# Performance work log

Measured on AMD Instinct MI355X. Metric: run time of the kernel, lower is better.

## Reference

```python
import jax, jax.numpy as jnp
import numpy as np

D = 768
H = 8
DH = D // H
SCALE = DH ** -0.5


def layer_norm(x, g, b, eps=1e-5):
    mu = jnp.mean(x, axis=-1, keepdims=True)
    var = jnp.var(x, axis=-1, keepdims=True)
    return (x - mu) * jax.lax.rsqrt(var + eps) * g + b


def setup_inputs() -> dict:
    key = jax.random.key(0)
    ks = jax.random.split(key, 8)
    B, N = 8, 1024
    s = lambda fan_in: 1.0 / np.sqrt(fan_in)
    return {
        "x": jax.random.normal(ks[0], (B, N, D), jnp.float32),
        "w_qkv": jax.random.normal(ks[1], (D, 3 * D), jnp.float32) * s(D),
        "w_o": jax.random.normal(ks[2], (D, D), jnp.float32) * s(D),
        "b_o": jnp.zeros((D,), jnp.float32),
        "w1": jax.random.normal(ks[3], (D, 4 * D), jnp.float32) * s(D),
        "b1": jnp.zeros((4 * D,), jnp.float32),
        "w2": jax.random.normal(ks[4], (4 * D, D), jnp.float32) * s(4 * D),
        "b2": jnp.zeros((D,), jnp.float32),
        "g1": jnp.ones((D,), jnp.float32), "be1": jnp.zeros((D,), jnp.float32),
        "gm": jnp.ones((D,), jnp.float32), "bm": jnp.zeros((D,), jnp.float32),
        "g3": jnp.ones((D,), jnp.float32), "be3": jnp.zeros((D,), jnp.float32),
    }


def reference(x, w_qkv, w_o, b_o, w1, b1, w2, b2, g1, be1, gm, bm, g3, be3):
    B, N, _ = x.shape
    # --- attention branch (pre-norm) ---
    h = layer_norm(x, g1, be1)
    qkv = h @ w_qkv                                   # (B,N,3D)
    qkv = qkv.reshape(B, N, 3, H, DH).transpose(2, 0, 3, 1, 4)  # (3,B,H,N,Dh)
    q, k, v = qkv[0], qkv[1], qkv[2]
    att = jax.nn.softmax(jnp.einsum('bhnd,bhmd->bhnm', q, k) * SCALE, axis=-1)
    o = jnp.einsum('bhnm,bhmd->bhnd', att, v)         # (B,H,N,Dh)
    # faithful to original: reshape WITHOUT transposing heads back
    o = o.reshape(B, N, D)
    o = o @ w_o + b_o
    x = o + x
    # --- MLP branch (has its own pre-norm; GELU after BOTH linears; dropout off) ---
    h = layer_norm(x, gm, bm)
    h = jax.nn.gelu(h @ w1 + b1, approximate=False)
    h = jax.nn.gelu(h @ w2 + b2, approximate=False)
    x = h + x
    return layer_norm(x, g3, be3)
```

## Files before the change

### kernel.cpp

```cpp
#include <hip/hip_runtime.h>
#include <cmath>
#include <cstdint>

typedef __bf16 bf16;
typedef __bf16 bf16x8 __attribute__((ext_vector_type(8)));
typedef __bf16 bf16x4 __attribute__((ext_vector_type(4)));
typedef float  f32x4  __attribute__((ext_vector_type(4)));

#define M_TOK 8192
#define SCALE_ 0.10206207261596575f

__device__ __forceinline__ void gld_lds16(const void* g, void* l) {
  __builtin_amdgcn_global_load_lds(
      (__attribute__((address_space(1))) void*)(uintptr_t)g,
      (__attribute__((address_space(3))) void*)(uintptr_t)l,
      16, 0, 0);
}

__device__ __forceinline__ float gelu_f(float x) {
  float u = x * (0.7978845608f + 0.0356774081f * x * x);
  float t = 1.0f - 2.0f / (__expf(2.0f * u) + 1.0f);
  return 0.5f * x * (1.0f + t);
}

__global__ __launch_bounds__(256) void make_frags_kernel(
    const float* __restrict__ w_qkv, const float* __restrict__ w_o,
    const float* __restrict__ w1, const float* __restrict__ w2,
    bf16* __restrict__ fqkv, bf16* __restrict__ fwo, bf16* __restrict__ fw1,
    bf16* __restrict__ fw2) {
  int chunk = blockIdx.x * 4 + (threadIdx.x >> 6);
  int lane = threadIdx.x & 63;
  const float* src;
  bf16* dst;
  int K, N, base;
  if (chunk < 3456) {
    src = w_qkv; dst = fqkv; K = 768; N = 2304; base = 0;
  } else if (chunk < 4608) {
    src = w_o; dst = fwo; K = 768; N = 768; base = 3456;
  } else if (chunk < 9216) {
    src = w1; dst = fw1; K = 768; N = 3072; base = 4608;
  } else {
    src = w2; dst = fw2; K = 3072; N = 768; base = 9216;
  }
  int lid = chunk - base;
  int kc = K / 32;
  int n16 = lid / kc, c = lid - n16 * kc;
  int lr = lane & 15, qd = lane >> 4;
  int n = n16 * 16 + lr;
  int k0 = c * 32 + qd * 8;
  bf16x8 v;
#pragma unroll
  for (int e = 0; e < 8; e++) v[e] = (bf16)src[(size_t)(k0 + e) * N + n];
  *(bf16x8*)&dst[(size_t)lid * 512 + lane * 8] = v;
}

__global__ __launch_bounds__(256) void ln_kernel(
    const float* __restrict__ x, const float* __restrict__ g,
    const float* __restrict__ b, bf16* __restrict__ ob) {
  int w = threadIdx.x >> 6, lane = threadIdx.x & 63;
  size_t row = (size_t)blockIdx.x * 4 + w;
  const float* xr = x + row * 768;
  float4 v[3];
  float s = 0.f, sq = 0.f;
#pragma unroll
  for (int k = 0; k < 3; k++) {
    v[k] = *(const float4*)(xr + (k * 64 + lane) * 4);
    s += v[k].x + v[k].y + v[k].z + v[k].w;
    sq += v[k].x * v[k].x + v[k].y * v[k].y + v[k].z * v[k].z + v[k].w * v[k].w;
  }
#pragma unroll
  for (int off = 32; off >= 1; off >>= 1) {
    s += __shfl_xor(s, off);
    sq += __shfl_xor(sq, off);
  }
  float mean = s * (1.f / 768.f);
  float rstd = rsqrtf(sq * (1.f / 768.f) - mean * mean + 1e-5f);
#pragma unroll
  for (int k = 0; k < 3; k++) {
    int c = (k * 64 + lane) * 4;
    float4 gg = *(const float4*)(g + c);
    float4 bb = *(const float4*)(b + c);
    bf16x4 pk = {(bf16)((v[k].x - mean) * rstd * gg.x + bb.x),
                 (bf16)((v[k].y - mean) * rstd * gg.y + bb.y),
                 (bf16)((v[k].z - mean) * rstd * gg.z + bb.z),
                 (bf16)((v[k].w - mean) * rstd * gg.w + bb.w)};
    *(bf16x4*)(ob + row * 768 + c) = pk;
  }
}

__global__ __launch_bounds__(256) void ln2_reduce_kernel(
    const bf16* __restrict__ p, const float* __restrict__ bo,
    const float* __restrict__ xres, const float* __restrict__ g,
    const float* __restrict__ b, bf16* __restrict__ x2,
    bf16* __restrict__ h2) {
  int w = threadIdx.x >> 6, lane = threadIdx.x & 63;
  size_t row = (size_t)blockIdx.x * 4 + w;
  const bf16* p0 = p + row * 768;
  const bf16* p1 = p0 + (size_t)M_TOK * 768;
  const float* xr = xres + row * 768;
  float4 v[3];
  float s = 0.f, sq = 0.f;
#pragma unroll
  for (int k = 0; k < 3; k++) {
    int c = (k * 64 + lane) * 4;
    bf16x4 a0 = *(const bf16x4*)(p0 + c);
    bf16x4 a1 = *(const bf16x4*)(p1 + c);
    float4 bb = *(const float4*)(bo + c);
    float4 rr = *(const float4*)(xr + c);
    v[k].x = (float)a0[0] + (float)a1[0] + bb.x + rr.x;
    v[k].y = (float)a0[1] + (float)a1[1] + bb.y + rr.y;
    v[k].z = (float)a0[2] + (float)a1[2] + bb.z + rr.z;
    v[k].w = (float)a0[3] + (float)a1[3] + bb.w + rr.w;
    bf16x4 xo = {(bf16)v[k].x, (bf16)v[k].y, (bf16)v[k].z, (bf16)v[k].w};
    *(bf16x4*)(x2 + row * 768 + c) = xo;
    s += v[k].x + v[k].y + v[k].z + v[k].w;
    sq += v[k].x * v[k].x + v[k].y * v[k].y + v[k].z * v[k].z + v[k].w * v[k].w;
  }
#pragma unroll
  for (int off = 32; off >= 1; off >>= 1) {
    s += __shfl_xor(s, off);
    sq += __shfl_xor(sq, off);
  }
  float mean = s * (1.f / 768.f);
  float rstd = rsqrtf(sq * (1.f / 768.f) - mean * mean + 1e-5f);
#pragma unroll
  for (int k = 0; k < 3; k++) {
    int c = (k * 64 + lane) * 4;
    float4 gg = *(const float4*)(g + c);
    float4 bb = *(const float4*)(b + c);
    bf16x4 pk = {(bf16)((v[k].x - mean) * rstd * gg.x + bb.x),
                 (bf16)((v[k].y - mean) * rstd * gg.y + bb.y),
                 (bf16)((v[k].z - mean) * rstd * gg.z + bb.z),
                 (bf16)((v[k].w - mean) * rstd * gg.w + bb.w)};
    *(bf16x4*)(h2 + row * 768 + c) = pk;
  }
}

__global__ __launch_bounds__(256) void ln3_reduce_kernel(
    const bf16* __restrict__ p, const float* __restrict__ b2,
    const bf16* __restrict__ x2, const float* __restrict__ g,
    const float* __restrict__ b, float* __restrict__ out) {
  int w = threadIdx.x >> 6, lane = threadIdx.x & 63;
  size_t row = (size_t)blockIdx.x * 4 + w;
  const bf16* p0 = p + row * 768;
  const bf16* p1 = p0 + (size_t)M_TOK * 768;
  const bf16* xr = x2 + row * 768;
  float4 v[3];
  float s = 0.f, sq = 0.f;
#pragma unroll
  for (int k = 0; k < 3; k++) {
    int c = (k * 64 + lane) * 4;
    bf16x4 a0 = *(const bf16x4*)(p0 + c);
    bf16x4 a1 = *(const bf16x4*)(p1 + c);
    float4 bb = *(const float4*)(b2 + c);
    bf16x4 rr = *(const bf16x4*)(xr + c);
    v[k].x = gelu_f((float)a0[0] + (float)a1[0] + bb.x) + (float)rr[0];
    v[k].y = gelu_f((float)a0[1] + (float)a1[1] + bb.y) + (float)rr[1];
    v[k].z = gelu_f((float)a0[2] + (float)a1[2] + bb.z) + (float)rr[2];
    v[k].w = gelu_f((float)a0[3] + (float)a1[3] + bb.w) + (float)rr[3];
    s += v[k].x + v[k].y + v[k].z + v[k].w;
    sq += v[k].x * v[k].x + v[k].y * v[k].y + v[k].z * v[k].z + v[k].w * v[k].w;
  }
#pragma unroll
  for (int off = 32; off >= 1; off >>= 1) {
    s += __shfl_xor(s, off);
    sq += __shfl_xor(sq, off);
  }
  float mean = s * (1.f / 768.f);
  float rstd = rsqrtf(sq * (1.f / 768.f) - mean * mean + 1e-5f);
#pragma unroll
  for (int k = 0; k < 3; k++) {
    int c = (k * 64 + lane) * 4;
    float4 gg = *(const float4*)(g + c);
    float4 bb = *(const float4*)(b + c);
    float4 ov = {(v[k].x - mean) * rstd * gg.x + bb.x,
                 (v[k].y - mean) * rstd * gg.y + bb.y,
                 (v[k].z - mean) * rstd * gg.z + bb.z,
                 (v[k].w - mean) * rstd * gg.w + bb.w};
    *(float4*)(out + row * 768 + c) = ov;
  }
}

template <int EPI, int LDA, int KTOT, int KSL, int NN>
__global__ __launch_bounds__(512, 2) void gemm8p_kernel(
    const bf16* __restrict__ A, const bf16* __restrict__ Bf,
    const float* __restrict__ bias, bf16* __restrict__ outb,
    bf16* __restrict__ qo, bf16* __restrict__ ko, bf16* __restrict__ vto) {
  constexpr int KCg = KTOT / 32;
  constexpr int NT = KSL / 64;
  __shared__ __align__(16) bf16 smem[3][24576];
  int tid = threadIdx.x;
  int w = tid >> 6, l = tid & 63;
  int qd = l >> 4, lr = l & 15;
  int bm0 = blockIdx.x * 128, bn0 = blockIdx.y * 256;
  int kbase = blockIdx.z * KSL;
  int wm = (w >> 2) * 64;
  int wnl = (w & 3) * 4;

  int rA = w * 8 + (l >> 3);
  int csA = (l & 7) ^ (l >> 3);
  const bf16* pA =
      A + (size_t)(bm0 + rA) * LDA + kbase + csA * 8;
  const bf16* pB0 =
      Bf + ((size_t)((bn0 >> 4) + (w >> 1)) * KCg + (kbase >> 5) + (w & 1)) *
               512 +
      l * 8;

  auto STG_A = [&](int t, bf16* buf) {
    gld_lds16(pA + t * 64, (char*)buf + w * 1024);
    gld_lds16(pA + t * 64 + (size_t)64 * LDA, (char*)buf + (8 + w) * 1024);
  };
  auto STG_B = [&](int t, bf16* buf, int g) {
    gld_lds16(pB0 + (size_t)g * (4 * KCg * 512) + (size_t)t * 1024,
              (char*)buf + 16384 + (w + 8 * g) * 1024);
  };

  STG_A(0, smem[0]);
  STG_B(0, smem[0], 0); STG_B(0, smem[0], 1);
  STG_B(0, smem[0], 2); STG_B(0, smem[0], 3);
  STG_A(1, smem[1]);
  STG_B(1, smem[1], 0); STG_B(1, smem[1], 1);
  STG_B(1, smem[1], 2); STG_B(1, smem[1], 3);
  asm volatile("s_waitcnt vmcnt(6)" ::: "memory");
  __builtin_amdgcn_sched_barrier(0);
  __builtin_amdgcn_s_barrier();

  f32x4 acc[4][4] = {};

#pragma unroll 1
  for (int kt3 = 0; kt3 < NT; kt3 += 3) {
#pragma unroll
    for (int u = 0; u < 3; ++u) {
      const int kt = kt3 + u;
      const bf16* Ab = smem[u];
      const bf16* Bb = smem[u] + 8192;
      bf16* nbuf = smem[(u + 2) % 3];
      bool st = (kt + 2) < NT;
#pragma unroll
      for (int k2 = 0; k2 < 2; ++k2) {
        bf16x8 af[4], bv[4];
        __builtin_amdgcn_sched_barrier(0);
#pragma unroll
        for (int i = 0; i < 4; ++i)
          af[i] = *(const bf16x8*)(Ab + (wm + i * 16 + lr) * 64 +
                                   (((k2 << 2) | qd) ^ (lr & 7)) * 8);
#pragma unroll
        for (int j = 0; j < 4; ++j)
          bv[j] = *(const bf16x8*)(Bb + (((wnl + j) << 1) | k2) * 512 + l * 8);
        __builtin_amdgcn_sched_barrier(0);
        if (k2 == 0) {
          if (st) { STG_A(kt + 2, nbuf); STG_B(kt + 2, nbuf, 0); }
        } else {
          if (st) {
            STG_B(kt + 2, nbuf, 1);
            STG_B(kt + 2, nbuf, 2);
            STG_B(kt + 2, nbuf, 3);
          }
        }
        __builtin_amdgcn_sched_barrier(0);
        __builtin_amdgcn_s_barrier();
        asm volatile("s_waitcnt lgkmcnt(0)" ::: "memory");
        __builtin_amdgcn_sched_barrier(0);
        __builtin_amdgcn_s_setprio(1);
#pragma unroll
        for (int i = 0; i < 4; ++i)
#pragma unroll
          for (int j = 0; j < 4; ++j)
            acc[i][j] = __builtin_amdgcn_mfma_f32_16x16x32_bf16(
                af[i], bv[j], acc[i][j], 0, 0, 0);
        __builtin_amdgcn_s_setprio(0);
        __builtin_amdgcn_sched_barrier(0);
      }
      if (kt + 1 < NT) {
        if (st) asm volatile("s_waitcnt vmcnt(6)" ::: "memory");
        else    asm volatile("s_waitcnt vmcnt(0)" ::: "memory");
        __builtin_amdgcn_sched_barrier(0);
        __builtin_amdgcn_s_barrier();
      }
    }
  }

  int wn = (w & 3) * 64;
  bf16* outbs = (EPI == 5) ? outb + (size_t)blockIdx.z * M_TOK * NN : outb;

#pragma unroll
  for (int i = 0; i < 4; i++) {
#pragma unroll
    for (int j = 0; j < 4; j++) {
      if (EPI == 4) {
        int colt = bn0 + wn + j * 16;
        int which = colt / 768;
        int rem = colt - which * 768;
        int h = rem / 96;
        int dhb = rem - h * 96;
        int row0 = bm0 + wm + i * 16 + qd * 4;
        int b = row0 >> 10, n0 = row0 & 1023;
        int bh = b * 8 + h;
        if (which == 2) {
          bf16x4 pk = {(bf16)acc[i][j][0], (bf16)acc[i][j][1],
                       (bf16)acc[i][j][2], (bf16)acc[i][j][3]};
          *(bf16x4*)(vto + ((size_t)(bh * 96 + dhb + lr)) * 1024 + n0) = pk;
        } else if (which == 0) {
#pragma unroll
          for (int r = 0; r < 4; r++)
            qo[((size_t)bh * 1024 + n0 + r) * 96 + dhb + lr] =
                (bf16)(acc[i][j][r] * SCALE_);
        } else {
#pragma unroll
          for (int r = 0; r < 4; r++)
            ko[((size_t)bh * 1024 + n0 + r) * 96 + dhb + lr] =
                (bf16)acc[i][j][r];
        }
      } else {
#pragma unroll
        for (int r = 0; r < 4; r++) {
          int row = bm0 + wm + i * 16 + qd * 4 + r;
          int col = bn0 + wn + j * 16 + lr;
          size_t o = (size_t)row * NN + col;
          float v = acc[i][j][r];
          if (EPI == 2) {
            outbs[o] = (bf16)gelu_f(v + bias[col]);
          } else {
            outbs[o] = (bf16)v;
          }
        }
      }
    }
  }
}

__global__ __launch_bounds__(256) void attn_kernel(
    const bf16* __restrict__ qb, const bf16* __restrict__ kb,
    const bf16* __restrict__ vtb, bf16* __restrict__ operm) {
  __shared__ __align__(16) bf16 Ks[2][64 * 104];
  __shared__ __align__(16) bf16 Vs[2][96 * 72];
  __shared__ __align__(16) bf16 Ps[128 * 72];
  int t = threadIdx.x;
  int w = t >> 6, lane = t & 63;
  int qd = lane >> 4, lr = lane & 15;
  int bh = blockIdx.x, nt0 = blockIdx.y * 128;
  int bq = bh >> 3, hh = bh & 7;

  const bf16* kgb = kb + (size_t)bh * 1024 * 96;
  const bf16* vgb = vtb + (size_t)bh * 96 * 1024;

  bf16x8 kreg[3], vreg[3];
#pragma unroll
  for (int it = 0; it < 3; it++) {
    int idx = it * 256 + t;
    kreg[it] = *(const bf16x8*)(kgb + (idx / 12) * 96 + (idx % 12) * 8);
    vreg[it] = *(const bf16x8*)(vgb + (size_t)(idx >> 3) * 1024 + (idx & 7) * 8);
  }

  const bf16* qg = qb + ((size_t)bh * 1024 + nt0 + w * 32) * 96;
  bf16x8 afq[2][3];
#pragma unroll
  for (int i = 0; i < 2; i++)
#pragma unroll
    for (int ks = 0; ks < 3; ks++)
      afq[i][ks] = *(const bf16x8*)(qg + (i * 16 + lr) * 96 + ks * 32 + qd * 8);

  f32x4 oacc[2][6] = {};
  float lst[2][4] = {};

  int cur = 0;
  for (int kt = 0; kt < 16; kt++) {
#pragma unroll
    for (int it = 0; it < 3; it++) {
      int idx = it * 256 + t;
      *(bf16x8*)&Ks[cur][(idx / 12) * 104 + (idx % 12) * 8] = kreg[it];
      *(bf16x8*)&Vs[cur][(idx >> 3) * 72 + (idx & 7) * 8] = vreg[it];
    }
    if (kt < 15) {
      const bf16* kg = kgb + (size_t)(kt + 1) * 64 * 96;
      const bf16* vg = vgb + (kt + 1) * 64;
#pragma unroll
      for (int it = 0; it < 3; it++) {
        int idx = it * 256 + t;
        kreg[it] = *(const bf16x8*)(kg + (idx / 12) * 96 + (idx % 12) * 8);
        vreg[it] =
            *(const bf16x8*)(vg + (size_t)(idx >> 3) * 1024 + (idx & 7) * 8);
      }
    }
    __syncthreads();

    f32x4 sacc[2][4] = {};
#pragma unroll
    for (int ks = 0; ks < 3; ks++) {
      bf16x8 bk[4];
#pragma unroll
      for (int jn = 0; jn < 4; jn++)
        bk[jn] =
            *(const bf16x8*)&Ks[cur][(jn * 16 + lr) * 104 + ks * 32 + qd * 8];
#pragma unroll
      for (int i = 0; i < 2; i++)
#pragma unroll
        for (int jn = 0; jn < 4; jn++)
          sacc[i][jn] = __builtin_amdgcn_mfma_f32_16x16x32_bf16(
              afq[i][ks], bk[jn], sacc[i][jn], 0, 0, 0);
    }

#pragma unroll
    for (int i = 0; i < 2; i++)
#pragma unroll
      for (int jn = 0; jn < 4; jn++)
#pragma unroll
        for (int r = 0; r < 4; r++) {
          float p = __expf(sacc[i][jn][r]);
          lst[i][r] += p;
          Ps[(w * 32 + i * 16 + qd * 4 + r) * 72 + jn * 16 + lr] = (bf16)p;
        }

#pragma unroll
    for (int ks = 0; ks < 2; ks++) {
      bf16x8 ap[2];
#pragma unroll
      for (int i = 0; i < 2; i++)
        ap[i] =
            *(const bf16x8*)&Ps[(w * 32 + i * 16 + lr) * 72 + ks * 32 + qd * 8];
#pragma unroll
      for (int jn = 0; jn < 6; jn++) {
        bf16x8 bv =
            *(const bf16x8*)&Vs[cur][(jn * 16 + lr) * 72 + ks * 32 + qd * 8];
#pragma unroll
        for (int i = 0; i < 2; i++)
          oacc[i][jn] = __builtin_amdgcn_mfma_f32_16x16x32_bf16(
              ap[i], bv, oacc[i][jn], 0, 0, 0);
      }
    }
    cur ^= 1;
  }

#pragma unroll
  for (int i = 0; i < 2; i++)
#pragma unroll
    for (int r = 0; r < 4; r++) {
#pragma unroll
      for (int off = 1; off < 16; off <<= 1)
        lst[i][r] += __shfl_xor(lst[i][r], off);
    }

#pragma unroll
  for (int i = 0; i < 2; i++) {
#pragma unroll
    for (int r = 0; r < 4; r++) {
      float inv = 1.0f / lst[i][r];
      int n = nt0 + w * 32 + i * 16 + qd * 4 + r;
      size_t rowo = (size_t)bq * 1024 + hh * 128 + (n >> 3);
      int colb = 96 * (n & 7);
#pragma unroll
      for (int jn = 0; jn < 6; jn++)
        operm[rowo * 768 + colb + jn * 16 + lr] =
            (bf16)(oacc[i][jn][r] * inv);
    }
  }
}

extern "C" void kernel_launch(void* const* d_in, const int* in_sizes, int n_in,
                              void* d_out, int out_size, void* d_ws,
                              size_t ws_size, hipStream_t stream) {
  const float* x = (const float*)d_in[0];
  const float* w_qkv = (const float*)d_in[1];
  const float* w_o = (const float*)d_in[2];
  const float* b_o = (const float*)d_in[3];
  const float* w1 = (const float*)d_in[4];
  const float* b1 = (const float*)d_in[5];
  const float* w2 = (const float*)d_in[6];
  const float* b2 = (const float*)d_in[7];
  const float* g1 = (const float*)d_in[8];
  const float* be1 = (const float*)d_in[9];
  const float* gm = (const float*)d_in[10];
  const float* bm = (const float*)d_in[11];
  const float* g3 = (const float*)d_in[12];
  const float* be3 = (const float*)d_in[13];

  char* ws = (char*)d_ws;
  size_t off = 0;
  auto alloc = [&](size_t bytes) {
    char* p = ws + off;
    off += (bytes + 255) & ~(size_t)255;
    return p;
  };
  const size_t SZ_TOK_BF = (size_t)M_TOK * 768 * 2;
  bf16* fqkv = (bf16*)alloc((size_t)2304 * 768 * 2);
  bf16* fwo = (bf16*)alloc((size_t)768 * 768 * 2);
  bf16* fw1 = (bf16*)alloc((size_t)3072 * 768 * 2);
  bf16* fw2 = (bf16*)alloc((size_t)768 * 3072 * 2);
  bf16* hA = (bf16*)alloc(SZ_TOK_BF);
  bf16* qb = (bf16*)alloc(SZ_TOK_BF);
  bf16* kbuf = (bf16*)alloc(SZ_TOK_BF);
  bf16* vtb = (bf16*)alloc(SZ_TOK_BF);
  bf16* x2 = (bf16*)alloc(SZ_TOK_BF);
  char* G = alloc((size_t)M_TOK * 3072 * 2);
  bf16* operm = hA;
  bf16* h2 = hA;
  bf16* pWo = (bf16*)G;
  bf16* a1 = (bf16*)G;
  bf16* pW2 = hA;

  make_frags_kernel<<<3456, 256, 0, stream>>>(w_qkv, w_o, w1, w2, fqkv, fwo,
                                              fw1, fw2);

  ln_kernel<<<M_TOK / 4, 256, 0, stream>>>(x, g1, be1, hA);

  gemm8p_kernel<4, 768, 768, 768, 2304><<<dim3(64, 9), 512, 0, stream>>>(
      hA, fqkv, nullptr, nullptr, qb, kbuf, vtb);

  attn_kernel<<<dim3(64, 8), 256, 0, stream>>>(qb, kbuf, vtb, operm);

  gemm8p_kernel<5, 768, 768, 384, 768><<<dim3(64, 3, 2), 512, 0, stream>>>(
      operm, fwo, nullptr, pWo, nullptr, nullptr, nullptr);

  ln2_reduce_kernel<<<M_TOK / 4, 256, 0, stream>>>(pWo, b_o, x, gm, bm, x2, h2);

  gemm8p_kernel<2, 768, 768, 768, 3072><<<dim3(64, 12), 512, 0, stream>>>(
      h2, fw1, b1, a1, nullptr, nullptr, nullptr);

  gemm8p_kernel<5, 3072, 3072, 1536, 768><<<dim3(64, 3, 2), 512, 0, stream>>>(
      a1, fw2, nullptr, pW2, nullptr, nullptr, nullptr);

  ln3_reduce_kernel<<<M_TOK / 4, 256, 0, stream>>>(pW2, b2, x2, g3, be3,
                                                   (float*)d_out);
}
```

Before: 361.1 us.

## Double-buffer LDS fragment registers to overlap ds_reads with MFMA in GEMM loop

Restructures the GEMM inner loop so the LDS-to-register fragment loads for the next k-half (and next tile's first half) are issued before the current MFMA block. This hides ds_read latency behind the matrix instructions. It also drops one of the two per-half-step barriers, using a partial lgkmcnt wait instead. The cost is doubled fragment registers, which could lower occupancy, plus subtler waitcnt correctness.

```diff
diff --git a/kernel.cpp b/kernel.cpp
--- a/kernel.cpp
+++ b/kernel.cpp
@@ -214,6 +214,17 @@
     gld_lds16(pB0 + (size_t)g * (4 * KCg * 512) + (size_t)t * 1024,
               (char*)buf + 16384 + (w + 8 * g) * 1024);
   };
+  auto LD_A = [&](const bf16* Ab, int k2, bf16x8* af) {
+#pragma unroll
+    for (int i = 0; i < 4; ++i)
+      af[i] = *(const bf16x8*)(Ab + (wm + i * 16 + lr) * 64 +
+                               (((k2 << 2) | qd) ^ (lr & 7)) * 8);
+  };
+  auto LD_B = [&](const bf16* Bb, int k2, bf16x8* bv) {
+#pragma unroll
+    for (int j = 0; j < 4; ++j)
+      bv[j] = *(const bf16x8*)(Bb + (((wnl + j) << 1) | k2) * 512 + l * 8);
+  };
 
   STG_A(0, smem[0]);
   STG_B(0, smem[0], 0); STG_B(0, smem[0], 1);
@@ -224,6 +235,12 @@
   asm volatile("s_waitcnt vmcnt(6)" ::: "memory");
   __builtin_amdgcn_sched_barrier(0);
   __builtin_amdgcn_s_barrier();
+  __builtin_amdgcn_sched_barrier(0);
+
+  bf16x8 aA[4], bA[4], aB[4], bB[4];
+  LD_A(smem[0], 0, aA);
+  LD_B(smem[0] + 8192, 0, bA);
+  __builtin_amdgcn_sched_barrier(0);
 
   f32x4 acc[4][4] = {};
 
@@ -234,49 +251,55 @@
       const int kt = kt3 + u;
       const bf16* Ab = smem[u];
       const bf16* Bb = smem[u] + 8192;
+      const bf16* Abn = smem[(u + 1) % 3];
+      const bf16* Bbn = smem[(u + 1) % 3] + 8192;
       bf16* nbuf = smem[(u + 2) % 3];
       bool st = (kt + 2) < NT;
-#pragma unroll
-      for (int k2 = 0; k2 < 2; ++k2) {
-        bf16x8 af[4], bv[4];
-        __builtin_amdgcn_sched_barrier(0);
-#pragma unroll
-        for (int i = 0; i < 4; ++i)
-          af[i] = *(const bf16x8*)(Ab + (wm + i * 16 + lr) * 64 +
-                                   (((k2 << 2) | qd) ^ (lr & 7)) * 8);
+      bool more = (kt + 1) < NT;
+
+      __builtin_amdgcn_sched_barrier(0);
+      LD_A(Ab, 1, aB);
+      LD_B(Bb, 1, bB);
+      __builtin_amdgcn_sched_barrier(0);
+      if (st) { STG_A(kt + 2, nbuf); STG_B(kt + 2, nbuf, 0); }
+      __builtin_amdgcn_sched_barrier(0);
+      asm volatile("s_waitcnt lgkmcnt(8)" ::: "memory");
+      __builtin_amdgcn_sched_barrier(0);
+      __builtin_amdgcn_s_setprio(1);
+#pragma unroll
+      for (int i = 0; i < 4; ++i)
 #pragma unroll
         for (int j = 0; j < 4; ++j)
-          bv[j] = *(const bf16x8*)(Bb + (((wnl + j) << 1) | k2) * 512 + l * 8);
-        __builtin_amdgcn_sched_barrier(0);
-        if (k2 == 0) {
-          if (st) { STG_A(kt + 2, nbuf); STG_B(kt + 2, nbuf, 0); }
-        } else {
-          if (st) {
-            STG_B(kt + 2, nbuf, 1);
-            STG_B(kt + 2, nbuf, 2);
-            STG_B(kt + 2, nbuf, 3);
-          }
-        }
-        __builtin_amdgcn_sched_barrier(0);
-        __builtin_amdgcn_s_barrier();
-        asm volatile("s_waitcnt lgkmcnt(0)" ::: "memory");
-        __builtin_amdgcn_sched_barrier(0);
-        __builtin_amdgcn_s_setprio(1);
-#pragma unroll
-        for (int i = 0; i < 4; ++i)
-#pragma unroll
-          for (int j = 0; j < 4; ++j)
-            acc[i][j] = __builtin_amdgcn_mfma_f32_16x16x32_bf16(
-                af[i], bv[j], acc[i][j], 0, 0, 0);
-        __builtin_amdgcn_s_setprio(0);
-        __builtin_amdgcn_sched_barrier(0);
+          acc[i][j] = __builtin_amdgcn_mfma_f32_16x16x32_bf16(
+              aA[i], bA[j], acc[i][j], 0, 0, 0);
+      __builtin_amdgcn_s_setprio(0);
+      __builtin_amdgcn_sched_barrier(0);
+
+      if (st) {
+        STG_B(kt + 2, nbuf, 1);
+        STG_B(kt + 2, nbuf, 2);
+        STG_B(kt + 2, nbuf, 3);
       }
-      if (kt + 1 < NT) {
-        if (st) asm volatile("s_waitcnt vmcnt(6)" ::: "memory");
-        else    asm volatile("s_waitcnt vmcnt(0)" ::: "memory");
-        __builtin_amdgcn_sched_barrier(0);
-        __builtin_amdgcn_s_barrier();
+      __builtin_amdgcn_sched_barrier(0);
+      if (st) asm volatile("s_waitcnt vmcnt(6) lgkmcnt(0)" ::: "memory");
+      else    asm volatile("s_waitcnt vmcnt(0) lgkmcnt(0)" ::: "memory");
+      __builtin_amdgcn_sched_barrier(0);
+      __builtin_amdgcn_s_barrier();
+      __builtin_amdgcn_sched_barrier(0);
+      if (more) {
+        LD_A(Abn, 0, aA);
+        LD_B(Bbn, 0, bA);
       }
+      __builtin_amdgcn_sched_barrier(0);
+      __builtin_amdgcn_s_setprio(1);
+#pragma unroll
+      for (int i = 0; i < 4; ++i)
+#pragma unroll
+        for (int j = 0; j < 4; ++j)
+          acc[i][j] = __builtin_amdgcn_mfma_f32_16x16x32_bf16(
+              aB[i], bB[j], acc[i][j], 0, 0, 0);
+      __builtin_amdgcn_s_setprio(0);
+      __builtin_amdgcn_sched_barrier(0);
     }
   }
 
```

Result: faster. 323.6 us (-10.4%).

## Enlarge GEMM tiles to 256x256 with double-buffered eight-phase pipeline

Applied to the files above, without the earlier changes.

Replaces the 128x256 triple-buffered GEMM with a 256x256 tile where each warp computes 128x64 outputs. Loads are interleaved across eight sub-phases over two LDS buffers, with A and B staged in halves. This is meant to raise arithmetic intensity and cut global/LDS traffic per FLOP. In exchange it doubles accumulator registers and LDS use per block and halves the number of workgroups, which may limit occupancy and leave CUs idle on the smaller GEMMs.

```diff
diff --git a/kernel.cpp b/kernel.cpp
--- a/kernel.cpp
+++ b/kernel.cpp
@@ -182,113 +182,215 @@
 }
 
 template <int EPI, int LDA, int KTOT, int KSL, int NN>
-__global__ __launch_bounds__(512, 2) void gemm8p_kernel(
+__global__ __launch_bounds__(512, 2) void gemm256_kernel(
     const bf16* __restrict__ A, const bf16* __restrict__ Bf,
     const float* __restrict__ bias, bf16* __restrict__ outb,
     bf16* __restrict__ qo, bf16* __restrict__ ko, bf16* __restrict__ vto) {
   constexpr int KCg = KTOT / 32;
   constexpr int NT = KSL / 64;
-  __shared__ __align__(16) bf16 smem[3][24576];
+  constexpr int NI = NT / 2;
+  __shared__ __align__(16) bf16 smem[2][32768];
   int tid = threadIdx.x;
   int w = tid >> 6, l = tid & 63;
   int qd = l >> 4, lr = l & 15;
-  int bm0 = blockIdx.x * 128, bn0 = blockIdx.y * 256;
+  int bm0 = blockIdx.x * 256, bn0 = blockIdx.y * 256;
   int kbase = blockIdx.z * KSL;
-  int wm = (w >> 2) * 64;
+  int wm = (w >> 2) * 128;
   int wnl = (w & 3) * 4;
-
-  int rA = w * 8 + (l >> 3);
-  int csA = (l & 7) ^ (l >> 3);
-  const bf16* pA =
-      A + (size_t)(bm0 + rA) * LDA + kbase + csA * 8;
-  const bf16* pB0 =
-      Bf + ((size_t)((bn0 >> 4) + (w >> 1)) * KCg + (kbase >> 5) + (w & 1)) *
-               512 +
-      l * 8;
-
-  auto STG_A = [&](int t, bf16* buf) {
-    gld_lds16(pA + t * 64, (char*)buf + w * 1024);
-    gld_lds16(pA + t * 64 + (size_t)64 * LDA, (char*)buf + (8 + w) * 1024);
+  int ah = wm >> 7;
+
+  const bf16* pA = A + (size_t)(bm0 + w * 8 + (l >> 3)) * LDA + kbase +
+                   ((l & 7) ^ (l >> 3)) * 8;
+  const bf16* pB =
+      Bf + ((size_t)((bn0 >> 4) + w) * KCg + (kbase >> 5)) * 512 + l * 8;
+
+  auto STG_A = [&](int t, int h, bf16* buf) {
+    const bf16* s = pA + (size_t)(h * 128) * LDA + t * 64;
+    bf16* d = buf + h * 8192 + w * 512;
+    gld_lds16(s, d);
+    gld_lds16(s + (size_t)64 * LDA, d + 4096);
   };
-  auto STG_B = [&](int t, bf16* buf, int g) {
-    gld_lds16(pB0 + (size_t)g * (4 * KCg * 512) + (size_t)t * 1024,
-              (char*)buf + 16384 + (w + 8 * g) * 1024);
+  auto STG_B = [&](int t, int h, bf16* buf) {
+    const bf16* s = pB + ((size_t)h * 8 * KCg + t * 2) * 512;
+    bf16* d = buf + 16384 + h * 8192 + w * 1024;
+    gld_lds16(s, d);
+    gld_lds16(s + 512, d + 512);
   };
-
-  STG_A(0, smem[0]);
-  STG_B(0, smem[0], 0); STG_B(0, smem[0], 1);
-  STG_B(0, smem[0], 2); STG_B(0, smem[0], 3);
-  STG_A(1, smem[1]);
-  STG_B(1, smem[1], 0); STG_B(1, smem[1], 1);
-  STG_B(1, smem[1], 2); STG_B(1, smem[1], 3);
-  asm volatile("s_waitcnt vmcnt(6)" ::: "memory");
+  auto LD_A4 = [&](const bf16* buf, int i0, int k2, bf16x8* af) {
+#pragma unroll
+    for (int i = 0; i < 4; ++i) {
+      int r = (i0 + i) * 16 + lr;
+      af[i] = *(const bf16x8*)(buf + ah * 8192 + r * 64 +
+                               ((k2 * 4 + qd) ^ (r & 7)) * 8);
+    }
+  };
+  auto LD_B4 = [&](const bf16* buf, int k2, bf16x8* bv) {
+#pragma unroll
+    for (int j = 0; j < 4; ++j) {
+      int n16 = wnl + j;
+      bv[j] = *(const bf16x8*)(buf + 16384 + (n16 >> 3) * 8192 +
+                               ((n16 & 7) * 2 + k2) * 512 + l * 8);
+    }
+  };
+
+  f32x4 acc[8][4] = {};
+  auto MM = [&](bf16x8* af, bf16x8* bv, int i0) {
+#pragma unroll
+    for (int i = 0; i < 4; ++i)
+#pragma unroll
+      for (int j = 0; j < 4; ++j)
+        acc[i0 + i][j] = __builtin_amdgcn_mfma_f32_16x16x32_bf16(
+            af[i], bv[j], acc[i0 + i][j], 0, 0, 0);
+  };
+
+  STG_A(0, 0, smem[0]); STG_A(0, 1, smem[0]);
+  STG_B(0, 0, smem[0]); STG_B(0, 1, smem[0]);
+  STG_B(1, 0, smem[1]);
+  asm volatile("s_waitcnt vmcnt(2)" ::: "memory");
   __builtin_amdgcn_sched_barrier(0);
   __builtin_amdgcn_s_barrier();
-
-  f32x4 acc[4][4] = {};
+  __builtin_amdgcn_sched_barrier(0);
+
+  bf16x8 af[4], bv[4];
 
 #pragma unroll 1
-  for (int kt3 = 0; kt3 < NT; kt3 += 3) {
-#pragma unroll
-    for (int u = 0; u < 3; ++u) {
-      const int kt = kt3 + u;
-      const bf16* Ab = smem[u];
-      const bf16* Bb = smem[u] + 8192;
-      bf16* nbuf = smem[(u + 2) % 3];
-      bool st = (kt + 2) < NT;
-#pragma unroll
-      for (int k2 = 0; k2 < 2; ++k2) {
-        bf16x8 af[4], bv[4];
-        __builtin_amdgcn_sched_barrier(0);
-#pragma unroll
-        for (int i = 0; i < 4; ++i)
-          af[i] = *(const bf16x8*)(Ab + (wm + i * 16 + lr) * 64 +
-                                   (((k2 << 2) | qd) ^ (lr & 7)) * 8);
-#pragma unroll
-        for (int j = 0; j < 4; ++j)
-          bv[j] = *(const bf16x8*)(Bb + (((wnl + j) << 1) | k2) * 512 + l * 8);
-        __builtin_amdgcn_sched_barrier(0);
-        if (k2 == 0) {
-          if (st) { STG_A(kt + 2, nbuf); STG_B(kt + 2, nbuf, 0); }
-        } else {
-          if (st) {
-            STG_B(kt + 2, nbuf, 1);
-            STG_B(kt + 2, nbuf, 2);
-            STG_B(kt + 2, nbuf, 3);
-          }
-        }
-        __builtin_amdgcn_sched_barrier(0);
-        __builtin_amdgcn_s_barrier();
-        asm volatile("s_waitcnt lgkmcnt(0)" ::: "memory");
-        __builtin_amdgcn_sched_barrier(0);
-        __builtin_amdgcn_s_setprio(1);
-#pragma unroll
-        for (int i = 0; i < 4; ++i)
-#pragma unroll
-          for (int j = 0; j < 4; ++j)
-            acc[i][j] = __builtin_amdgcn_mfma_f32_16x16x32_bf16(
-                af[i], bv[j], acc[i][j], 0, 0, 0);
-        __builtin_amdgcn_s_setprio(0);
-        __builtin_amdgcn_sched_barrier(0);
-      }
-      if (kt + 1 < NT) {
-        if (st) asm volatile("s_waitcnt vmcnt(6)" ::: "memory");
-        else    asm volatile("s_waitcnt vmcnt(0)" ::: "memory");
-        __builtin_amdgcn_sched_barrier(0);
-        __builtin_amdgcn_s_barrier();
-      }
-    }
-  }
-
-  int wn = (w & 3) * 64;
+  for (int it = 0; it < NI; ++it) {
+    const int T = 2 * it;
+    bf16* b0 = smem[0];
+    bf16* b1 = smem[1];
+    const bool s2 = (it + 1 < NI);
+
+    __builtin_amdgcn_sched_barrier(0);
+    LD_B4(b0, 0, bv);
+    LD_A4(b0, 0, 0, af);
+    __builtin_amdgcn_sched_barrier(0);
+    STG_A(T + 1, 0, b1);
+    __builtin_amdgcn_sched_barrier(0);
+    __builtin_amdgcn_s_barrier();
+    asm volatile("s_waitcnt lgkmcnt(0)" ::: "memory");
+    __builtin_amdgcn_sched_barrier(0);
+    __builtin_amdgcn_s_setprio(1);
+    MM(af, bv, 0);
+    __builtin_amdgcn_s_setprio(0);
+    __builtin_amdgcn_sched_barrier(0);
+    __builtin_amdgcn_s_barrier();
+
+    __builtin_amdgcn_sched_barrier(0);
+    LD_A4(b0, 4, 0, af);
+    __builtin_amdgcn_sched_barrier(0);
+    STG_A(T + 1, 1, b1);
+    __builtin_amdgcn_sched_barrier(0);
+    __builtin_amdgcn_s_barrier();
+    asm volatile("s_waitcnt lgkmcnt(0)" ::: "memory");
+    __builtin_amdgcn_sched_barrier(0);
+    __builtin_amdgcn_s_setprio(1);
+    MM(af, bv, 4);
+    __builtin_amdgcn_s_setprio(0);
+    __builtin_amdgcn_sched_barrier(0);
+    __builtin_amdgcn_s_barrier();
+
+    __builtin_amdgcn_sched_barrier(0);
+    LD_B4(b0, 1, bv);
+    LD_A4(b0, 0, 1, af);
+    __builtin_amdgcn_sched_barrier(0);
+    STG_B(T + 1, 1, b1);
+    __builtin_amdgcn_sched_barrier(0);
+    __builtin_amdgcn_s_barrier();
+    asm volatile("s_waitcnt lgkmcnt(0)" ::: "memory");
+    __builtin_amdgcn_sched_barrier(0);
+    __builtin_amdgcn_s_setprio(1);
+    MM(af, bv, 0);
+    __builtin_amdgcn_s_setprio(0);
+    __builtin_amdgcn_sched_barrier(0);
+    __builtin_amdgcn_s_barrier();
+
+    __builtin_amdgcn_sched_barrier(0);
+    LD_A4(b0, 4, 1, af);
+    __builtin_amdgcn_sched_barrier(0);
+    if (s2) STG_B(T + 2, 0, b0);
+    __builtin_amdgcn_sched_barrier(0);
+    __builtin_amdgcn_s_barrier();
+    asm volatile("s_waitcnt lgkmcnt(0)" ::: "memory");
+    __builtin_amdgcn_sched_barrier(0);
+    __builtin_amdgcn_s_setprio(1);
+    MM(af, bv, 4);
+    __builtin_amdgcn_s_setprio(0);
+    __builtin_amdgcn_sched_barrier(0);
+    if (s2) asm volatile("s_waitcnt vmcnt(2)" ::: "memory");
+    else    asm volatile("s_waitcnt vmcnt(0)" ::: "memory");
+    __builtin_amdgcn_sched_barrier(0);
+    __builtin_amdgcn_s_barrier();
+
+    __builtin_amdgcn_sched_barrier(0);
+    LD_B4(b1, 0, bv);
+    LD_A4(b1, 0, 0, af);
+    __builtin_amdgcn_sched_barrier(0);
+    if (s2) STG_A(T + 2, 0, b0);
+    __builtin_amdgcn_sched_barrier(0);
+    __builtin_amdgcn_s_barrier();
+    asm volatile("s_waitcnt lgkmcnt(0)" ::: "memory");
+    __builtin_amdgcn_sched_barrier(0);
+    __builtin_amdgcn_s_setprio(1);
+    MM(af, bv, 0);
+    __builtin_amdgcn_s_setprio(0);
+    __builtin_amdgcn_sched_barrier(0);
+    __builtin_amdgcn_s_barrier();
+
+    __builtin_amdgcn_sched_barrier(0);
+    LD_A4(b1, 4, 0, af);
+    __builtin_amdgcn_sched_barrier(0);
+    if (s2) STG_A(T + 2, 1, b0);
+    __builtin_amdgcn_sched_barrier(0);
+    __builtin_amdgcn_s_barrier();
+    asm volatile("s_waitcnt lgkmcnt(0)" ::: "memory");
+    __builtin_amdgcn_sched_barrier(0);
+    __builtin_amdgcn_s_setprio(1);
+    MM(af, bv, 4);
+    __builtin_amdgcn_s_setprio(0);
+    __builtin_amdgcn_sched_barrier(0);
+    __builtin_amdgcn_s_barrier();
+
+    __builtin_amdgcn_sched_barrier(0);
+    LD_B4(b1, 1, bv);
+    LD_A4(b1, 0, 1, af);
+    __builtin_amdgcn_sched_barrier(0);
+    if (s2) STG_B(T + 2, 1, b0);
+    __builtin_amdgcn_sched_barrier(0);
+    __builtin_amdgcn_s_barrier();
+    asm volatile("s_waitcnt lgkmcnt(0)" ::: "memory");
+    __builtin_amdgcn_sched_barrier(0);
+    __builtin_amdgcn_s_setprio(1);
+    MM(af, bv, 0);
+    __builtin_amdgcn_s_setprio(0);
+    __builtin_amdgcn_sched_barrier(0);
+    __builtin_amdgcn_s_barrier();
+
+    __builtin_amdgcn_sched_barrier(0);
+    LD_A4(b1, 4, 1, af);
+    __builtin_amdgcn_sched_barrier(0);
+    if (s2) STG_B(T + 3, 0, b1);
+    __builtin_amdgcn_sched_barrier(0);
+    __builtin_amdgcn_s_barrier();
+    asm volatile("s_waitcnt lgkmcnt(0)" ::: "memory");
+    __builtin_amdgcn_sched_barrier(0);
+    __builtin_amdgcn_s_setprio(1);
+    MM(af, bv, 4);
+    __builtin_amdgcn_s_setprio(0);
+    __builtin_amdgcn_sched_barrier(0);
+    if (s2) asm volatile("s_waitcnt vmcnt(2)" ::: "memory");
+    else    asm volatile("s_waitcnt vmcnt(0)" ::: "memory");
+    __builtin_amdgcn_sched_barrier(0);
+    __builtin_amdgcn_s_barrier();
+  }
+
   bf16* outbs = (EPI == 5) ? outb + (size_t)blockIdx.z * M_TOK * NN : outb;
 
 #pragma unroll
-  for (int i = 0; i < 4; i++) {
+  for (int i = 0; i < 8; i++) {
 #pragma unroll
     for (int j = 0; j < 4; j++) {
       if (EPI == 4) {
-        int colt = bn0 + wn + j * 16;
+        int colt = bn0 + (wnl + j) * 16;
         int which = colt / 768;
         int rem = colt - which * 768;
         int h = rem / 96;
@@ -315,7 +417,7 @@
 #pragma unroll
         for (int r = 0; r < 4; r++) {
           int row = bm0 + wm + i * 16 + qd * 4 + r;
-          int col = bn0 + wn + j * 16 + lr;
+          int col = bn0 + (wnl + j) * 16 + lr;
           size_t o = (size_t)row * NN + col;
           float v = acc[i][j][r];
           if (EPI == 2) {
@@ -503,20 +605,20 @@
 
   ln_kernel<<<M_TOK / 4, 256, 0, stream>>>(x, g1, be1, hA);
 
-  gemm8p_kernel<4, 768, 768, 768, 2304><<<dim3(64, 9), 512, 0, stream>>>(
+  gemm256_kernel<4, 768, 768, 768, 2304><<<dim3(32, 9), 512, 0, stream>>>(
       hA, fqkv, nullptr, nullptr, qb, kbuf, vtb);
 
   attn_kernel<<<dim3(64, 8), 256, 0, stream>>>(qb, kbuf, vtb, operm);
 
-  gemm8p_kernel<5, 768, 768, 384, 768><<<dim3(64, 3, 2), 512, 0, stream>>>(
+  gemm256_kernel<5, 768, 768, 384, 768><<<dim3(32, 3, 2), 512, 0, stream>>>(
       operm, fwo, nullptr, pWo, nullptr, nullptr, nullptr);
 
   ln2_reduce_kernel<<<M_TOK / 4, 256, 0, stream>>>(pWo, b_o, x, gm, bm, x2, h2);
 
-  gemm8p_kernel<2, 768, 768, 768, 3072><<<dim3(64, 12), 512, 0, stream>>>(
+  gemm256_kernel<2, 768, 768, 768, 3072><<<dim3(32, 12), 512, 0, stream>>>(
       h2, fw1, b1, a1, nullptr, nullptr, nullptr);
 
-  gemm8p_kernel<5, 3072, 3072, 1536, 768><<<dim3(64, 3, 2), 512, 0, stream>>>(
+  gemm256_kernel<5, 3072, 3072, 1536, 768><<<dim3(32, 3, 2), 512, 0, stream>>>(
       a1, fw2, nullptr, pW2, nullptr, nullptr, nullptr);
 
   ln3_reduce_kernel<<<M_TOK / 4, 256, 0, stream>>>(pW2, b2, x2, g3, be3,
```

New measurement: 358.0 us. About the same (-0.8%).
